# Optimization experiments

Hardware: AMD Instinct MI355X
Metric: run time of the kernel (lower is better)

The kernel has to match this reference:

```python
import jax, jax.numpy as jnp
import numpy as np
from jax import lax

NUM_HEADS = 8
EPS_BN = 1e-5
EPS_LN = 1e-5


def setup_inputs() -> dict:
    key = jax.random.key(0)
    ks = iter(jax.random.split(key, 32))
    C = 512
    R = C // 16  # channel-gate reduction
    HID = 512    # classifier hidden
    NC = 1       # num_classes

    def gn(shape, scale=0.02):
        return (jax.random.normal(next(ks), shape, dtype=jnp.float32) * scale)

    inp = {
        "x": jax.random.normal(next(ks), (16, C, 28, 28), dtype=jnp.float32),
        # ChannelGate MLP (Linear(C,R) -> ReLU -> Linear(R,C))
        "mlp_w1": gn((R, C)), "mlp_b1": jnp.zeros((R,), jnp.float32),
        "mlp_w2": gn((C, R)), "mlp_b2": jnp.zeros((C,), jnp.float32),
        # SpatialGate 7x7 conv (2->1, no bias) + BatchNorm2d(1) eval-mode stats
        "sp_w": gn((1, 2, 7, 7)),
        "sp_gamma": jnp.ones((1,), jnp.float32), "sp_beta": jnp.zeros((1,), jnp.float32),
        "sp_mean": jnp.zeros((1,), jnp.float32), "sp_var": jnp.ones((1,), jnp.float32),
        # attention projections
        "wq": gn((C, C)), "bq": jnp.zeros((C,), jnp.float32),
        "wk": gn((C, C)), "bk": jnp.zeros((C,), jnp.float32),
        "wv": gn((C, C)), "bv": jnp.zeros((C,), jnp.float32),
        "wo": gn((C, C)), "bo": jnp.zeros((C,), jnp.float32),
        # classifier: LayerNorm(C) -> Linear(C,512) -> ReLU -> Linear(512,NC)
        "ln_g": jnp.ones((C,), jnp.float32), "ln_b": jnp.zeros((C,), jnp.float32),
        "fc1_w": gn((HID, C)), "fc1_b": jnp.zeros((HID,), jnp.float32),
        "fc2_w": gn((NC, HID)), "fc2_b": jnp.zeros((NC,), jnp.float32),
    }
    return inp


def reference(x, mlp_w1, mlp_b1, mlp_w2, mlp_b2, sp_w, sp_gamma, sp_beta,
              sp_mean, sp_var, wq, bq, wk, bk, wv, bv, wo, bo,
              ln_g, ln_b, fc1_w, fc1_b, fc2_w, fc2_b):
    B, C, H, W = x.shape
    N = H * W
    hd = C // NUM_HEADS

    # ---- CBAM: channel gate (avg + max global pools through shared MLP) ----
    def mlp(p):  # p: [B, C]
        return jax.nn.relu(p @ mlp_w1.T + mlp_b1) @ mlp_w2.T + mlp_b2

    avg_p = x.mean(axis=(2, 3))
    max_p = x.max(axis=(2, 3))
    ch_scale = jax.nn.sigmoid(mlp(avg_p) + mlp(max_p))[:, :, None, None]
    x = x * ch_scale

    # ---- CBAM: spatial gate ----
    comp = jnp.concatenate([x.max(axis=1, keepdims=True),
                            x.mean(axis=1, keepdims=True)], axis=1)  # [B,2,H,W]
    s = lax.conv_general_dilated(comp, sp_w, window_strides=(1, 1),
                                 padding=[(3, 3), (3, 3)],
                                 dimension_numbers=("NCHW", "OIHW", "NCHW"))
    s = (s - sp_mean[None, :, None, None]) * lax.rsqrt(sp_var + EPS_BN)[None, :, None, None]
    s = s * sp_gamma[None, :, None, None] + sp_beta[None, :, None, None]
    x = x * jax.nn.sigmoid(s)

    # ---- multi-head self-attention over HW tokens ----
    xf = x.reshape(B, C, N).transpose(0, 2, 1)  # [B, N, C]

    def heads(w, b):
        return (xf @ w.T + b).reshape(B, N, NUM_HEADS, hd).transpose(0, 2, 1, 3)

    Q, K, V = heads(wq, bq), heads(wk, bk), heads(wv, bv)  # [B, h, N, d]
    scores = jnp.einsum("bhnd,bhmd->bhnm", Q, K) / jnp.sqrt(jnp.float32(hd))
    attn = jax.nn.softmax(scores, axis=-1)  # dropout is identity in eval
    attended = jnp.einsum("bhnm,bhmd->bhnd", attn, V)
    attended = attended.transpose(0, 2, 1, 3).reshape(B, N, C)
    attended = attended @ wo.T + bo
    x = x + attended.transpose(0, 2, 1).reshape(B, C, H, W)

    # ---- classifier head ----
    p = x.mean(axis=(2, 3))  # AdaptiveAvgPool2d(1) + Flatten -> [B, C]
    mu = p.mean(axis=-1, keepdims=True)
    var = p.var(axis=-1, keepdims=True)
    ln = (p - mu) * lax.rsqrt(var + EPS_LN) * ln_g + ln_b
    h = jax.nn.relu(ln @ fc1_w.T + fc1_b)
    return h @ fc2_w.T + fc2_b
```

## Files before the change

### kernel.cpp

```cpp
#include <hip/hip_runtime.h>
#include <math.h>

#define BB 16
#define CC 512
#define HW 784
#define RR 32
#define NHD 8
#define HD 64
#define NT 784
#define NTILE 49
#define CBS 132

#define OFS_AVGP   0
#define OFS_MAXP   8192
#define OFS_CHS    16384
#define OFS_SP     49664
#define OFS_P1     62208
#define OFS_ABAR   70400
#define OFS_XG     78592
#define XG_SZ      (BB*CC*HW)
#define OFS_XGT    (OFS_XG + XG_SZ)
#define OFS_QBF    (OFS_XGT + XG_SZ/2)
#define OFS_KBF    (OFS_QBF + XG_SZ/2)
#define OFS_V2     (OFS_KBF + XG_SZ/2)
#define OFS_WF     (OFS_V2 + XG_SZ)
#define OFS_W      OFS_XG
#define OFS_PV     (OFS_XG + 131072)
#define OFS_CMAXP  (OFS_XG + 262144)
#define OFS_CMEANP (OFS_CMAXP + 200704)

typedef __attribute__((ext_vector_type(8))) short bf16x8;
typedef __attribute__((ext_vector_type(4))) float f32x4;

__device__ __forceinline__ unsigned short f2bf(float x) {
  union { float f; unsigned u; } v; v.f = x;
  unsigned r = v.u + 0x7fffu + ((v.u >> 16) & 1u);
  return (unsigned short)(r >> 16);
}
__device__ __forceinline__ float bf2f(unsigned short x) {
  union { unsigned u; float f; } v; v.u = ((unsigned)x) << 16;
  return v.f;
}
__device__ __forceinline__ void async16(const unsigned short* g, unsigned short* l) {
  __builtin_amdgcn_global_load_lds(
      (const __attribute__((address_space(1))) unsigned int*)g,
      (__attribute__((address_space(3))) unsigned int*)l, 16, 0, 0);
}

__global__ void k_pre(const float* __restrict__ x,
                      const float* __restrict__ wq, const float* __restrict__ wk,
                      const float* __restrict__ wv,
                      float* avg_p, float* max_p, unsigned short* __restrict__ Wf,
                      float* __restrict__ wsum, float* __restrict__ p1,
                      float* __restrict__ outp) {
  int bid = blockIdx.x;
  if (bid < 2048) {
    int wid = threadIdx.x >> 6;
    int lane = threadIdx.x & 63;
    int row = bid * 4 + wid;
    const float* xr = x + (size_t)row * HW;
    float s = 0.f, m = -INFINITY;
    for (int i = lane; i < HW; i += 64) { float v = xr[i]; s += v; m = fmaxf(m, v); }
    for (int o = 32; o; o >>= 1) { s += __shfl_down(s, o, 64); m = fmaxf(m, __shfl_down(m, o, 64)); }
    if (lane == 0) { avg_p[row] = s * (1.f/HW); max_p[row] = m; }
  } else if (bid < 2432) {
    int idx = (bid - 2048)*256 + threadIdx.x;
    int ln = idx & 63;
    int s  = (idx >> 6) & 15;
    int ct = (idx >> 10) & 31;
    int mat = idx >> 15;
    const float* W = (mat==0)? wq : (mat==1)? wk : wv;
    const float* src = W + (size_t)(ct*16 + (ln & 15))*CC + s*32 + (ln >> 4)*8;
    float4 f0 = *(const float4*)src;
    float4 f1 = *(const float4*)(src + 4);
    bf16x8 p;
    p[0]=(short)f2bf(f0.x); p[1]=(short)f2bf(f0.y); p[2]=(short)f2bf(f0.z); p[3]=(short)f2bf(f0.w);
    p[4]=(short)f2bf(f1.x); p[5]=(short)f2bf(f1.y); p[6]=(short)f2bf(f1.z); p[7]=(short)f2bf(f1.w);
    *(bf16x8*)(Wf + (size_t)idx*8) = p;
  } else {
    int idx = (bid - 2432)*256 + threadIdx.x;
    const float4 z = {0.f,0.f,0.f,0.f};
    if (idx < 4) *(float4*)&outp[idx*4] = z;
    for (int i = idx; i < 27136; i += 16384) {
      if (i < 25088) *(float4*)&wsum[(size_t)i*4] = z;
      else           *(float4*)&p1[(size_t)(i-25088)*4] = z;
    }
  }
}

__global__ void k_chmlp(const float* avg_p, const float* max_p,
                        const float* w1, const float* b1,
                        const float* w2, const float* b2, float* chs) {
  __shared__ float pa[CC], pm[CC], part[256], hr[64];
  int b = blockIdx.x, t = threadIdx.x;
  for (int i = t; i < CC; i += 256) { pa[i] = avg_p[b*CC+i]; pm[i] = max_p[b*CC+i]; }
  __syncthreads();
  {
    int rp = t & 63, ch = t >> 6;
    int r = rp & 31;
    const float* src = (rp < 32) ? pa : pm;
    const float* wr = w1 + (size_t)r*CC + ch*128;
    float s = 0.f;
    #pragma unroll 8
    for (int c = 0; c < 128; c++) s += src[ch*128 + c] * wr[c];
    part[t] = s;
  }
  __syncthreads();
  if (t < 64)
    hr[t] = fmaxf(part[t] + part[64+t] + part[128+t] + part[192+t] + b1[t & 31], 0.f);
  __syncthreads();
  for (int c = t; c < CC; c += 256) {
    float a = 2.f*b2[c];
    const float* wr = w2 + c*RR;
    #pragma unroll
    for (int r = 0; r < RR; r++) a += (hr[r]+hr[32+r])*wr[r];
    chs[b*CC+c] = 1.f/(1.f+__expf(-a));
  }
}

__global__ void k_chgatep(const float* __restrict__ x, const float* __restrict__ chs,
                          float* __restrict__ cmaxp, float* __restrict__ cmeanp) {
  __shared__ float cs[32];
  int b = blockIdx.x, cg = blockIdx.y, t = threadIdx.x;
  if (t < 32) cs[t] = chs[b*CC + cg*32 + t];
  __syncthreads();
  const float* xb = x + ((size_t)b*CC + cg*32)*HW;
  for (int pix = t; pix < HW; pix += 256) {
    float mx = -INFINITY, sm = 0.f;
    #pragma unroll
    for (int c = 0; c < 32; c++) {
      float v = xb[(size_t)c*HW + pix] * cs[c];
      mx = fmaxf(mx, v); sm += v;
    }
    cmaxp[(size_t)(cg*BB + b)*HW + pix] = mx;
    cmeanp[(size_t)(cg*BB + b)*HW + pix] = sm;
  }
}

__global__ void k_credsp(const float* __restrict__ cmaxp, const float* __restrict__ cmeanp,
                         const float* __restrict__ w, const float* g, const float* be,
                         const float* mu, const float* var, float* __restrict__ sp) {
  __shared__ float cmx[HW], cmn[HW];
  int b = blockIdx.x, q = blockIdx.y, t = threadIdx.x;
  for (int pix = t; pix < HW; pix += 256) {
    float mx = -INFINITY, sm = 0.f;
    #pragma unroll
    for (int cg = 0; cg < 16; cg++) {
      mx = fmaxf(mx, cmaxp[(size_t)(cg*BB + b)*HW + pix]);
      sm += cmeanp[(size_t)(cg*BB + b)*HW + pix];
    }
    cmx[pix] = mx; cmn[pix] = sm * (1.f/CC);
  }
  __syncthreads();
  if (t < 196) {
    int pix = q*196 + t;
    float bnscale = rsqrtf(var[0]+1e-5f)*g[0];
    int h = pix/28, wd = pix%28;
    float acc = 0.f;
    for (int kh = 0; kh < 7; kh++) {
      int ih = h + kh - 3; if (ih < 0 || ih >= 28) continue;
      for (int kw = 0; kw < 7; kw++) {
        int iw = wd + kw - 3; if (iw < 0 || iw >= 28) continue;
        int ip = ih*28+iw;
        acc += cmx[ip]*w[kh*7+kw] + cmn[ip]*w[49+kh*7+kw];
      }
    }
    float s = (acc - mu[0])*bnscale + be[0];
    sp[b*HW+pix] = 1.f/(1.f+__expf(-s));
  }
}

__global__ void k_sfuse(const float* __restrict__ x, const float* __restrict__ chs,
                        const float* __restrict__ sp, unsigned short* __restrict__ xgT,
                        float* __restrict__ p1) {
  __shared__ float cs[CC];
  int nt = blockIdx.x, b = blockIdx.y;
  int t = threadIdx.x, ln = t & 63;
  for (int i = t; i < CC; i += 256) cs[i] = chs[b*CC+i];
  __syncthreads();
  int n = nt*16 + (ln & 15);
  float spv = sp[b*HW + n];
  const float* xb = x + (size_t)b*CC*HW;
  #pragma unroll
  for (int i = 0; i < 4; i++) {
    int s = (t >> 6) + 4*i;
    int c = s*32 + (ln >> 4)*8;
    float vf[8];
    bf16x8 p;
    #pragma unroll
    for (int j = 0; j < 8; j++) {
      vf[j] = xb[(size_t)(c+j)*HW + n] * cs[c+j] * spv;
      p[j] = (short)f2bf(vf[j]);
    }
    *(bf16x8*)(xgT + ((((size_t)b*NTILE + nt)*16 + s)*64 + ln)*8) = p;
    #pragma unroll
    for (int j = 0; j < 8; j++) {
      float v = vf[j];
      v += __shfl_xor(v,1,64); v += __shfl_xor(v,2,64);
      v += __shfl_xor(v,4,64); v += __shfl_xor(v,8,64);
      vf[j] = v;
    }
    if ((ln & 15) == 0) {
      #pragma unroll
      for (int j = 0; j < 8; j++) atomicAdd(&p1[b*CC + c + j], vf[j]);
    }
  }
}

__global__ __launch_bounds__(256) void k_qkv_mfma(
    const unsigned short* __restrict__ xgT, const unsigned short* __restrict__ Wf,
    const float* __restrict__ bq, const float* __restrict__ bk, const float* __restrict__ bv,
    unsigned short* __restrict__ Qbf, unsigned short* __restrict__ Kbf,
    unsigned short* __restrict__ Vbf) {
  __shared__ __align__(16) unsigned char smem[65536];
  unsigned short* Alds = (unsigned short*)smem;
  float* Cb = (float*)smem;
  int blk = blockIdx.x;
  int yb = blk / 208;
  int r0 = blk % 208;
  int mt = r0 >> 4;
  int b  = r0 & 15;
  int mat = yb >> 1;
  int c0 = (yb & 1) * 256;
  int t = threadIdx.x, w = t >> 6, ln = t & 63;
  const unsigned short* Ab = xgT + (size_t)b*NTILE*8192;
  const unsigned short* Bb = Wf + (size_t)mat*32*8192;
  int ctgb = (c0 >> 4) + w*2;
  int ntc[4];
  #pragma unroll
  for (int m = 0; m < 4; m++) { int nt = 4*mt + m; ntc[m] = (nt > 48) ? 48 : nt; }
  #pragma unroll
  for (int j0 = 0; j0 < 16; j0++) {
    int j = w + 4*j0;
    int m = j >> 4, sj = j & 15;
    async16(Ab + (size_t)ntc[m]*8192 + (size_t)(sj*64 + ln)*8,
            Alds + (size_t)j*512);
  }
  f32x4 acc[4][4];
  #pragma unroll
  for (int m = 0; m < 4; m++)
    #pragma unroll
    for (int c2 = 0; c2 < 4; c2++) acc[m][c2] = (f32x4){0.f,0.f,0.f,0.f};
  __syncthreads();
  #pragma unroll 2
  for (int s = 0; s < 16; s++) {
    bf16x8 bf[4];
    bf[0] = *(const bf16x8*)(Bb + (size_t)((ctgb  )*16 + s)*512 + ln*8);
    bf[1] = *(const bf16x8*)(Bb + (size_t)((ctgb+1)*16 + s)*512 + ln*8);
    bf[2] = *(const bf16x8*)(Bb + (size_t)((ctgb+8)*16 + s)*512 + ln*8);
    bf[3] = *(const bf16x8*)(Bb + (size_t)((ctgb+9)*16 + s)*512 + ln*8);
    bf16x8 af[4];
    #pragma unroll
    for (int m = 0; m < 4; m++)
      af[m] = *(const bf16x8*)(Alds + (size_t)(m*16 + s)*512 + ln*8);
    #pragma unroll
    for (int m = 0; m < 4; m++) {
      #pragma unroll
      for (int c2 = 0; c2 < 4; c2++)
        acc[m][c2] = __builtin_amdgcn_mfma_f32_16x16x32_bf16(af[m], bf[c2], acc[m][c2], 0,0,0);
    }
  }
  __syncthreads();
  const float* bias = (mat==0)? bq : (mat==1)? bk : bv;
  #pragma unroll
  for (int ch = 0; ch < 2; ch++) {
    if (ch) __syncthreads();
    #pragma unroll
    for (int m = 0; m < 4; m++)
      #pragma unroll
      for (int c2 = 0; c2 < 2; c2++)
        #pragma unroll
        for (int r = 0; r < 4; r++)
          Cb[(m*16 + (ln>>4)*4 + r)*CBS + w*32 + c2*16 + (ln&15)] = acc[m][ch*2+c2][r];
    __syncthreads();
    #pragma unroll
    for (int i = 0; i < 4; i++) {
      int p = w*4 + i;
      int ntl = p >> 2, sl = p & 3;
      int nt = 4*mt + ntl;
      if (nt > 48) continue;
      int row = ntl*16 + (ln & 15);
      int col = sl*32 + (ln >> 4)*8;
      float4 v0 = *(const float4*)&Cb[row*CBS + col];
      float4 v1 = *(const float4*)&Cb[row*CBS + col + 4];
      float v[8] = {v0.x, v0.y, v0.z, v0.w, v1.x, v1.y, v1.z, v1.w};
      int colA = ch*128 + col;
      #pragma unroll
      for (int j = 0; j < 8; j++) v[j] += bias[c0 + colA + j];
      int token = nt*16 + (ln & 15);
      int h = (c0 >> 6) + (ch << 1) + (sl >> 1);
      int bh = b*NHD + h;
      bf16x8 pk;
      #pragma unroll
      for (int j = 0; j < 8; j++) pk[j] = (short)f2bf(v[j]);
      if (mat < 2) {
        unsigned short* Out = (mat == 0) ? Qbf : Kbf;
        *(bf16x8*)(Out + ((size_t)bh*NTILE + nt)*1024 + (size_t)(sl & 1)*512 + ln*8) = pk;
      } else {
        int d = (sl & 1)*32 + (ln >> 4)*8;
        *(bf16x8*)(Vbf + ((size_t)bh*NT + token)*HD + d) = pk;
      }
    }
  }
}

__global__ __launch_bounds__(256, 3) void k_attn8(const unsigned short* __restrict__ Qbf,
    const unsigned short* __restrict__ Kbf, float* __restrict__ wsum) {
  __shared__ float l_tmp[2][64];
  __shared__ float rl[2][16];
  int bh = blockIdx.x & 127, pg = blockIdx.x >> 7;
  int t = threadIdx.x, w = t >> 6, ln = t & 63;
  int ntA = pg*2;
  bool hasB = (ntA + 1) < NTILE;
  int ntB = hasB ? (ntA + 1) : ntA;
  const unsigned short* QbA = Qbf + ((size_t)bh*NTILE + ntA)*1024;
  const unsigned short* QbB = Qbf + ((size_t)bh*NTILE + ntB)*1024;
  const unsigned short* Kb = Kbf + (size_t)bh*NTILE*1024;
  bf16x8 qA0 = *(const bf16x8*)(QbA + ln*8);
  bf16x8 qA1 = *(const bf16x8*)(QbA + 512 + ln*8);
  bf16x8 qB0 = *(const bf16x8*)(QbB + ln*8);
  bf16x8 qB1 = *(const bf16x8*)(QbB + 512 + ln*8);
  f32x4 evA[13], evB[13];
  float lpA[4] = {0.f,0.f,0.f,0.f}, lpB[4] = {0.f,0.f,0.f,0.f};
  #pragma unroll
  for (int i = 0; i < 13; i++) {
    int mt = w + 4*i;
    bool valid = (i < 12) || (w == 0);
    int mtc = valid ? mt : 48;
    bf16x8 k0 = *(const bf16x8*)(Kb + (size_t)mtc*1024 + ln*8);
    bf16x8 k1 = *(const bf16x8*)(Kb + (size_t)mtc*1024 + 512 + ln*8);
    f32x4 a = {0.f,0.f,0.f,0.f};
    a = __builtin_amdgcn_mfma_f32_16x16x32_bf16(qA0, k0, a, 0,0,0);
    a = __builtin_amdgcn_mfma_f32_16x16x32_bf16(qA1, k1, a, 0,0,0);
    f32x4 c = {0.f,0.f,0.f,0.f};
    c = __builtin_amdgcn_mfma_f32_16x16x32_bf16(qB0, k0, c, 0,0,0);
    c = __builtin_amdgcn_mfma_f32_16x16x32_bf16(qB1, k1, c, 0,0,0);
    f32x4 ea, eb;
    #pragma unroll
    for (int r = 0; r < 4; r++) {
      ea[r] = __expf(a[r]*0.125f);
      eb[r] = __expf(c[r]*0.125f);
    }
    evA[i] = ea; evB[i] = eb;
    if (valid) {
      #pragma unroll
      for (int r = 0; r < 4; r++) { lpA[r] += ea[r]; lpB[r] += eb[r]; }
    }
  }
  #pragma unroll
  for (int r = 0; r < 4; r++) {
    float v = lpA[r];
    v += __shfl_xor(v,1,64); v += __shfl_xor(v,2,64);
    v += __shfl_xor(v,4,64); v += __shfl_xor(v,8,64);
    if ((ln & 15) == 0) l_tmp[0][w*16 + (ln>>4)*4 + r] = v;
    float u = lpB[r];
    u += __shfl_xor(u,1,64); u += __shfl_xor(u,2,64);
    u += __shfl_xor(u,4,64); u += __shfl_xor(u,8,64);
    if ((ln & 15) == 0) l_tmp[1][w*16 + (ln>>4)*4 + r] = u;
  }
  __syncthreads();
  if (t < 32) {
    int g = t >> 4, q = t & 15;
    rl[g][q] = 1.f / (l_tmp[g][q] + l_tmp[g][16+q] + l_tmp[g][32+q] + l_tmp[g][48+q]);
  }
  __syncthreads();
  f32x4 rlA = *(const f32x4*)&rl[0][(ln >> 4)*4];
  f32x4 rlB = *(const f32x4*)&rl[1][(ln >> 4)*4];
  #pragma unroll
  for (int i = 0; i < 13; i++) {
    int mt = w + 4*i;
    bool valid = (i < 12) || (w == 0);
    float v = evA[i][0]*rlA[0] + evA[i][1]*rlA[1] + evA[i][2]*rlA[2] + evA[i][3]*rlA[3];
    if (hasB)
      v += evB[i][0]*rlB[0] + evB[i][1]*rlB[1] + evB[i][2]*rlB[2] + evB[i][3]*rlB[3];
    v += __shfl_xor(v, 16, 64);
    v += __shfl_xor(v, 32, 64);
    if (valid && ln < 16)
      atomicAdd(&wsum[bh*NT + mt*16 + ln], v);
  }
}

__global__ void k_attn_av(const float* __restrict__ w, const unsigned short* __restrict__ Vm,
                          float* __restrict__ abar) {
  __shared__ float red[256];
  int bh = blockIdx.x, t = threadIdx.x;
  int d = t & 63, chunk = t >> 6;
  float acc = 0.f;
  const unsigned short* vb = Vm + (size_t)bh*NT*HD;
  const float* wb = w + bh*NT;
  for (int m = chunk*196; m < (chunk+1)*196; m++)
    acc += wb[m] * bf2f(vb[(size_t)m*HD + d]);
  red[t] = acc;
  __syncthreads();
  if (t < 64)
    abar[bh*HD + t] = (red[t] + red[64+t] + red[128+t] + red[192+t]) * (1.f/NT);
}

__global__ void k_headA(const float* __restrict__ p1, const float* __restrict__ abar,
                        const float* __restrict__ wo, const float* __restrict__ bo,
                        float* __restrict__ pv) {
  int b = blockIdx.x, cg = blockIdx.y;
  int t = threadIdx.x, w = t >> 6, ln = t & 63;
  float a[8];
  #pragma unroll
  for (int k = 0; k < 8; k++) a[k] = abar[b*CC + ln + 64*k];
  int c0 = cg*32 + w*8;
  for (int i = 0; i < 8; i++) {
    int c = c0 + i;
    const float* wr = wo + (size_t)c*CC;
    float s = 0.f;
    #pragma unroll
    for (int k = 0; k < 8; k++) s += a[k] * wr[ln + 64*k];
    for (int o = 32; o; o >>= 1) s += __shfl_down(s, o, 64);
    if (ln == 0) pv[b*CC + c] = s + bo[c] + p1[b*CC + c] * (1.f/HW);
  }
}

__global__ void k_headC(const float* __restrict__ pv, const float* __restrict__ ln_g,
                        const float* __restrict__ ln_b, const float* __restrict__ fc1_w,
                        const float* __restrict__ fc1_b, const float* __restrict__ fc2_w,
                        const float* __restrict__ fc2_b, float* __restrict__ out) {
  int b = blockIdx.x, cg = blockIdx.y;
  int t = threadIdx.x, w = t >> 6, ln = t & 63;
  float a[8];
  float s = 0.f, s2 = 0.f;
  #pragma unroll
  for (int k = 0; k < 8; k++) {
    a[k] = pv[b*CC + ln + 64*k];
    s += a[k]; s2 += a[k]*a[k];
  }
  for (int o = 32; o; o >>= 1) { s += __shfl_down(s, o, 64); s2 += __shfl_down(s2, o, 64); }
  s = __shfl(s, 0, 64); s2 = __shfl(s2, 0, 64);
  float mean = s * (1.f/CC);
  float rs = rsqrtf(s2*(1.f/CC) - mean*mean + 1e-5f);
  #pragma unroll
  for (int k = 0; k < 8; k++)
    a[k] = (a[k]-mean)*rs*ln_g[ln + 64*k] + ln_b[ln + 64*k];
  int c0 = cg*32 + w*8;
  float o2 = 0.f;
  for (int i = 0; i < 8; i++) {
    int c = c0 + i;
    const float* wr = fc1_w + (size_t)c*CC;
    float v = 0.f;
    #pragma unroll
    for (int k = 0; k < 8; k++) v += a[k] * wr[ln + 64*k];
    for (int o = 32; o; o >>= 1) v += __shfl_down(v, o, 64);
    if (ln == 0) o2 += fmaxf(v + fc1_b[c], 0.f) * fc2_w[c];
  }
  if (ln == 0) {
    if (cg == 0 && w == 0) o2 += fc2_b[0];
    atomicAdd(&out[b], o2);
  }
}

extern "C" void kernel_launch(void* const* d_in, const int* in_sizes, int n_in,
                              void* d_out, int out_size, void* d_ws, size_t ws_size,
                              hipStream_t stream) {
  const float* x       = (const float*)d_in[0];
  const float* mlp_w1  = (const float*)d_in[1];
  const float* mlp_b1  = (const float*)d_in[2];
  const float* mlp_w2  = (const float*)d_in[3];
  const float* mlp_b2  = (const float*)d_in[4];
  const float* sp_w    = (const float*)d_in[5];
  const float* sp_g    = (const float*)d_in[6];
  const float* sp_b    = (const float*)d_in[7];
  const float* sp_mu   = (const float*)d_in[8];
  const float* sp_var  = (const float*)d_in[9];
  const float* wq      = (const float*)d_in[10];
  const float* bq      = (const float*)d_in[11];
  const float* wk      = (const float*)d_in[12];
  const float* bk      = (const float*)d_in[13];
  const float* wv      = (const float*)d_in[14];
  const float* bv      = (const float*)d_in[15];
  const float* wo      = (const float*)d_in[16];
  const float* bo      = (const float*)d_in[17];
  const float* ln_g    = (const float*)d_in[18];
  const float* ln_b    = (const float*)d_in[19];
  const float* fc1_w   = (const float*)d_in[20];
  const float* fc1_b   = (const float*)d_in[21];
  const float* fc2_w   = (const float*)d_in[22];
  const float* fc2_b   = (const float*)d_in[23];

  float* ws = (float*)d_ws;
  float* avg_p = ws + OFS_AVGP;
  float* max_p = ws + OFS_MAXP;
  float* chs   = ws + OFS_CHS;
  float* sp    = ws + OFS_SP;
  float* p1    = ws + OFS_P1;
  float* abar  = ws + OFS_ABAR;
  unsigned short* xgT = (unsigned short*)(ws + OFS_XGT);
  unsigned short* Qbf = (unsigned short*)(ws + OFS_QBF);
  unsigned short* Kbf = (unsigned short*)(ws + OFS_KBF);
  unsigned short* Vbf = (unsigned short*)(ws + OFS_V2);
  unsigned short* Wf  = (unsigned short*)(ws + OFS_WF);
  float* wsum  = ws + OFS_W;
  float* pv    = ws + OFS_PV;
  float* cmaxp = ws + OFS_CMAXP;
  float* cmeanp= ws + OFS_CMEANP;

  k_pre    <<<2496, 256, 0, stream>>>(x, wq, wk, wv, avg_p, max_p, Wf, wsum, p1,
                                      (float*)d_out);
  k_chmlp  <<<BB, 256, 0, stream>>>(avg_p, max_p, mlp_w1, mlp_b1, mlp_w2, mlp_b2, chs);
  k_chgatep<<<dim3(BB,16), 256, 0, stream>>>(x, chs, cmaxp, cmeanp);
  k_credsp <<<dim3(BB,4), 256, 0, stream>>>(cmaxp, cmeanp, sp_w, sp_g, sp_b, sp_mu, sp_var, sp);
  k_sfuse  <<<dim3(NTILE,BB), 256, 0, stream>>>(x, chs, sp, xgT, p1);
  k_qkv_mfma<<<1248, 256, 0, stream>>>(xgT, Wf, bq, bk, bv, Qbf, Kbf, Vbf);
  k_attn8  <<<25*128, 256, 0, stream>>>(Qbf, Kbf, wsum);
  k_attn_av<<<128, 256, 0, stream>>>(wsum, Vbf, abar);
  k_headA  <<<dim3(BB,16), 256, 0, stream>>>(p1, abar, wo, bo, pv);
  k_headC  <<<dim3(BB,16), 256, 0, stream>>>(pv, ln_g, ln_b, fc1_w, fc1_b,
                                             fc2_w, fc2_b, (float*)d_out);
}
```

Measured before the change: 276.9 us.

## Fuse channel MLP into gating, widen QKV blocks, split attn_av reduction

Merges the channel-gate MLP into the channel-gating pass, so each block recomputes the small MLP for its 32 channels and one launch goes away. The QKV MFMA kernel now runs 512 threads per block, with each wave computing half as many output column tiles, to raise per-block parallelism. The attention-weighted V reduction is split across 4x more blocks using atomics into abar, which is now zeroed in the prelude; the 1/NT scale moves to the consumer. The attn8 block index mapping is also reordered so the blocks for one head are adjacent. The cost is redundant MLP work per block and extra atomics.

Result: no change. 279.7 us (+1.0%).

```diff
diff --git a/kernel.cpp b/kernel.cpp
--- a/kernel.cpp
+++ b/kernel.cpp
@@ -81,18 +81,21 @@
     int idx = (bid - 2432)*256 + threadIdx.x;
     const float4 z = {0.f,0.f,0.f,0.f};
     if (idx < 4) *(float4*)&outp[idx*4] = z;
-    for (int i = idx; i < 27136; i += 16384) {
+    for (int i = idx; i < 29184; i += 16384) {
       if (i < 25088) *(float4*)&wsum[(size_t)i*4] = z;
       else           *(float4*)&p1[(size_t)(i-25088)*4] = z;
     }
   }
 }
 
-__global__ void k_chmlp(const float* avg_p, const float* max_p,
-                        const float* w1, const float* b1,
-                        const float* w2, const float* b2, float* chs) {
-  __shared__ float pa[CC], pm[CC], part[256], hr[64];
-  int b = blockIdx.x, t = threadIdx.x;
+__global__ void k_chgate2(const float* __restrict__ x,
+                          const float* __restrict__ avg_p, const float* __restrict__ max_p,
+                          const float* __restrict__ w1, const float* __restrict__ b1,
+                          const float* __restrict__ w2, const float* __restrict__ b2,
+                          float* __restrict__ chs,
+                          float* __restrict__ cmaxp, float* __restrict__ cmeanp) {
+  __shared__ float pa[CC], pm[CC], part[256], hr[64], cs[32];
+  int b = blockIdx.x, cg = blockIdx.y, t = threadIdx.x;
   for (int i = t; i < CC; i += 256) { pa[i] = avg_p[b*CC+i]; pm[i] = max_p[b*CC+i]; }
   __syncthreads();
   {
@@ -109,20 +112,16 @@
   if (t < 64)
     hr[t] = fmaxf(part[t] + part[64+t] + part[128+t] + part[192+t] + b1[t & 31], 0.f);
   __syncthreads();
-  for (int c = t; c < CC; c += 256) {
+  if (t < 32) {
+    int c = cg*32 + t;
     float a = 2.f*b2[c];
     const float* wr = w2 + c*RR;
     #pragma unroll
     for (int r = 0; r < RR; r++) a += (hr[r]+hr[32+r])*wr[r];
-    chs[b*CC+c] = 1.f/(1.f+__expf(-a));
-  }
-}
-
-__global__ void k_chgatep(const float* __restrict__ x, const float* __restrict__ chs,
-                          float* __restrict__ cmaxp, float* __restrict__ cmeanp) {
-  __shared__ float cs[32];
-  int b = blockIdx.x, cg = blockIdx.y, t = threadIdx.x;
-  if (t < 32) cs[t] = chs[b*CC + cg*32 + t];
+    float v = 1.f/(1.f+__expf(-a));
+    cs[t] = v;
+    chs[b*CC + c] = v;
+  }
   __syncthreads();
   const float* xb = x + ((size_t)b*CC + cg*32)*HW;
   for (int pix = t; pix < HW; pix += 256) {
@@ -207,7 +206,7 @@
   }
 }
 
-__global__ __launch_bounds__(256) void k_qkv_mfma(
+__global__ __launch_bounds__(512) void k_qkv_mfma(
     const unsigned short* __restrict__ xgT, const unsigned short* __restrict__ Wf,
     const float* __restrict__ bq, const float* __restrict__ bk, const float* __restrict__ bv,
     unsigned short* __restrict__ Qbf, unsigned short* __restrict__ Kbf,
@@ -222,42 +221,39 @@
   int b  = r0 & 15;
   int mat = yb >> 1;
   int c0 = (yb & 1) * 256;
-  int t = threadIdx.x, w = t >> 6, ln = t & 63;
+  int t = threadIdx.x, w8 = t >> 6, ln = t & 63;
+  int g = w8 >> 2, wq = w8 & 3;
   const unsigned short* Ab = xgT + (size_t)b*NTILE*8192;
   const unsigned short* Bb = Wf + (size_t)mat*32*8192;
-  int ctgb = (c0 >> 4) + w*2;
+  int cb = (c0 >> 4) + g*8 + wq*2;
   int ntc[4];
   #pragma unroll
   for (int m = 0; m < 4; m++) { int nt = 4*mt + m; ntc[m] = (nt > 48) ? 48 : nt; }
   #pragma unroll
-  for (int j0 = 0; j0 < 16; j0++) {
-    int j = w + 4*j0;
+  for (int j0 = 0; j0 < 8; j0++) {
+    int j = w8 + 8*j0;
     int m = j >> 4, sj = j & 15;
     async16(Ab + (size_t)ntc[m]*8192 + (size_t)(sj*64 + ln)*8,
             Alds + (size_t)j*512);
   }
-  f32x4 acc[4][4];
+  f32x4 acc[4][2];
   #pragma unroll
   for (int m = 0; m < 4; m++)
     #pragma unroll
-    for (int c2 = 0; c2 < 4; c2++) acc[m][c2] = (f32x4){0.f,0.f,0.f,0.f};
+    for (int c2 = 0; c2 < 2; c2++) acc[m][c2] = (f32x4){0.f,0.f,0.f,0.f};
   __syncthreads();
   #pragma unroll 2
   for (int s = 0; s < 16; s++) {
-    bf16x8 bf[4];
-    bf[0] = *(const bf16x8*)(Bb + (size_t)((ctgb  )*16 + s)*512 + ln*8);
-    bf[1] = *(const bf16x8*)(Bb + (size_t)((ctgb+1)*16 + s)*512 + ln*8);
-    bf[2] = *(const bf16x8*)(Bb + (size_t)((ctgb+8)*16 + s)*512 + ln*8);
-    bf[3] = *(const bf16x8*)(Bb + (size_t)((ctgb+9)*16 + s)*512 + ln*8);
+    bf16x8 bf0 = *(const bf16x8*)(Bb + (size_t)((cb  )*16 + s)*512 + ln*8);
+    bf16x8 bf1 = *(const bf16x8*)(Bb + (size_t)((cb+1)*16 + s)*512 + ln*8);
     bf16x8 af[4];
     #pragma unroll
     for (int m = 0; m < 4; m++)
       af[m] = *(const bf16x8*)(Alds + (size_t)(m*16 + s)*512 + ln*8);
     #pragma unroll
     for (int m = 0; m < 4; m++) {
-      #pragma unroll
-      for (int c2 = 0; c2 < 4; c2++)
-        acc[m][c2] = __builtin_amdgcn_mfma_f32_16x16x32_bf16(af[m], bf[c2], acc[m][c2], 0,0,0);
+      acc[m][0] = __builtin_amdgcn_mfma_f32_16x16x32_bf16(af[m], bf0, acc[m][0], 0,0,0);
+      acc[m][1] = __builtin_amdgcn_mfma_f32_16x16x32_bf16(af[m], bf1, acc[m][1], 0,0,0);
     }
   }
   __syncthreads();
@@ -265,17 +261,19 @@
   #pragma unroll
   for (int ch = 0; ch < 2; ch++) {
     if (ch) __syncthreads();
-    #pragma unroll
-    for (int m = 0; m < 4; m++)
+    if (g == ch) {
       #pragma unroll
-      for (int c2 = 0; c2 < 2; c2++)
+      for (int m = 0; m < 4; m++)
         #pragma unroll
-        for (int r = 0; r < 4; r++)
-          Cb[(m*16 + (ln>>4)*4 + r)*CBS + w*32 + c2*16 + (ln&15)] = acc[m][ch*2+c2][r];
+        for (int c2 = 0; c2 < 2; c2++)
+          #pragma unroll
+          for (int r = 0; r < 4; r++)
+            Cb[(m*16 + (ln>>4)*4 + r)*CBS + wq*32 + c2*16 + (ln&15)] = acc[m][c2][r];
+    }
     __syncthreads();
     #pragma unroll
-    for (int i = 0; i < 4; i++) {
-      int p = w*4 + i;
+    for (int i = 0; i < 2; i++) {
+      int p = w8*2 + i;
       int ntl = p >> 2, sl = p & 3;
       int nt = 4*mt + ntl;
       if (nt > 48) continue;
@@ -308,7 +306,7 @@
     const unsigned short* __restrict__ Kbf, float* __restrict__ wsum) {
   __shared__ float l_tmp[2][64];
   __shared__ float rl[2][16];
-  int bh = blockIdx.x & 127, pg = blockIdx.x >> 7;
+  int bh = blockIdx.x / 25, pg = blockIdx.x % 25;
   int t = threadIdx.x, w = t >> 6, ln = t & 63;
   int ntA = pg*2;
   bool hasB = (ntA + 1) < NTILE;
@@ -383,17 +381,19 @@
 __global__ void k_attn_av(const float* __restrict__ w, const unsigned short* __restrict__ Vm,
                           float* __restrict__ abar) {
   __shared__ float red[256];
-  int bh = blockIdx.x, t = threadIdx.x;
-  int d = t & 63, chunk = t >> 6;
+  int bh = blockIdx.x >> 2, qt = blockIdx.x & 3;
+  int t = threadIdx.x;
+  int d = t & 63, sub = t >> 6;
   float acc = 0.f;
   const unsigned short* vb = Vm + (size_t)bh*NT*HD;
   const float* wb = w + bh*NT;
-  for (int m = chunk*196; m < (chunk+1)*196; m++)
+  int m0 = qt*196 + sub*49;
+  for (int m = m0; m < m0 + 49; m++)
     acc += wb[m] * bf2f(vb[(size_t)m*HD + d]);
   red[t] = acc;
   __syncthreads();
   if (t < 64)
-    abar[bh*HD + t] = (red[t] + red[64+t] + red[128+t] + red[192+t]) * (1.f/NT);
+    atomicAdd(&abar[bh*HD + t], red[t] + red[64+t] + red[128+t] + red[192+t]);
 }
 
 __global__ void k_headA(const float* __restrict__ p1, const float* __restrict__ abar,
@@ -403,7 +403,7 @@
   int t = threadIdx.x, w = t >> 6, ln = t & 63;
   float a[8];
   #pragma unroll
-  for (int k = 0; k < 8; k++) a[k] = abar[b*CC + ln + 64*k];
+  for (int k = 0; k < 8; k++) a[k] = abar[b*CC + ln + 64*k] * (1.f/NT);
   int c0 = cg*32 + w*8;
   for (int i = 0; i < 8; i++) {
     int c = c0 + i;
@@ -500,13 +500,13 @@
 
   k_pre    <<<2496, 256, 0, stream>>>(x, wq, wk, wv, avg_p, max_p, Wf, wsum, p1,
                                       (float*)d_out);
-  k_chmlp  <<<BB, 256, 0, stream>>>(avg_p, max_p, mlp_w1, mlp_b1, mlp_w2, mlp_b2, chs);
-  k_chgatep<<<dim3(BB,16), 256, 0, stream>>>(x, chs, cmaxp, cmeanp);
+  k_chgate2<<<dim3(BB,16), 256, 0, stream>>>(x, avg_p, max_p, mlp_w1, mlp_b1,
+                                             mlp_w2, mlp_b2, chs, cmaxp, cmeanp);
   k_credsp <<<dim3(BB,4), 256, 0, stream>>>(cmaxp, cmeanp, sp_w, sp_g, sp_b, sp_mu, sp_var, sp);
   k_sfuse  <<<dim3(NTILE,BB), 256, 0, stream>>>(x, chs, sp, xgT, p1);
-  k_qkv_mfma<<<1248, 256, 0, stream>>>(xgT, Wf, bq, bk, bv, Qbf, Kbf, Vbf);
+  k_qkv_mfma<<<1248, 512, 0, stream>>>(xgT, Wf, bq, bk, bv, Qbf, Kbf, Vbf);
   k_attn8  <<<25*128, 256, 0, stream>>>(Qbf, Kbf, wsum);
-  k_attn_av<<<128, 256, 0, stream>>>(wsum, Vbf, abar);
+  k_attn_av<<<512, 256, 0, stream>>>(wsum, Vbf, abar);
   k_headA  <<<dim3(BB,16), 256, 0, stream>>>(p1, abar, wo, bo, pv);
   k_headC  <<<dim3(BB,16), 256, 0, stream>>>(pv, ln_g, ln_b, fc1_w, fc1_b,
                                              fc2_w, fc2_b, (float*)d_out);
```
